# Kernel optimization log

Hardware: AMD Instinct MI355X
Metric: run time of the kernel (lower is better)

The kernel has to match this reference:

```python
import jax, jax.numpy as jnp
import numpy as np

EMBED = 64
ATT_FACTOR = 10
N_FIELDS = 50
BATCH = 2048


def setup_inputs() -> dict:
    key = jax.random.key(0)
    k_x, k_w, k_h, k_p = jax.random.split(key, 4)
    x = jax.random.normal(k_x, (BATCH, N_FIELDS, EMBED), dtype=jnp.float32)
    # xavier-normal-ish init for params
    attention_W = jax.random.normal(k_w, (EMBED, ATT_FACTOR), dtype=jnp.float32) * (2.0 / (EMBED + ATT_FACTOR)) ** 0.5
    attention_b = jnp.zeros((ATT_FACTOR,), dtype=jnp.float32)
    projection_h = jax.random.normal(k_h, (ATT_FACTOR, 1), dtype=jnp.float32) * (2.0 / (ATT_FACTOR + 1)) ** 0.5
    projection_p = jax.random.normal(k_p, (EMBED, 1), dtype=jnp.float32) * (2.0 / (EMBED + 1)) ** 0.5
    return {"x": x, "attention_W": attention_W, "attention_b": attention_b,
            "projection_h": projection_h, "projection_p": projection_p}


def reference(x, attention_W, attention_b, projection_h, projection_p):
    F_ = x.shape[1]
    idx_i, idx_j = np.triu_indices(F_, k=1)  # all pairs (i<j), P = F*(F-1)/2
    inter = x[:, idx_i, :] * x[:, idx_j, :]  # [B, P, E]
    att_tmp = jax.nn.relu(jnp.einsum('bpe,ef->bpf', inter, attention_W) + attention_b)  # [B,P,A]
    logits = jnp.einsum('bpf,fo->bpo', att_tmp, projection_h)  # [B,P,1]
    score = jax.nn.softmax(logits, axis=1)  # softmax over pairs
    att_out = jnp.sum(score * inter, axis=1)  # [B, E]
    # dropout is identity at inference
    return att_out @ projection_p  # [B, 1]
```

## Files before the change

kernel.cpp:

```cpp
#include <hip/hip_runtime.h>
#include <math.h>


#define F_ 50
#define E_ 64
#define A_ 10
#define XDIM 64
#define XSTR 72
#define NT 384

typedef _Float16 half8 __attribute__((ext_vector_type(8)));
typedef _Float16 half4t __attribute__((ext_vector_type(4)));
typedef float f32x16 __attribute__((ext_vector_type(16)));

__global__ __launch_bounds__(NT, 2)
void afm_mfma_kernel(const float* __restrict__ x,
                     const float* __restrict__ W,
                     const float* __restrict__ bias,
                     const float* __restrict__ h,
                     const float* __restrict__ pp,
                     float* __restrict__ out, int nbatch) {
  __shared__ __align__(16) _Float16 sXh[2 * XDIM * XSTR];
  __shared__ __align__(16) _Float16 sWh[(A_ + 1) * E_];
  __shared__ float sb[A_], sh[A_];
  __shared__ float rn[6], rd[6];

  const int tid = threadIdx.x;
  const int b0 = blockIdx.x * 2;

  for (int q = tid; q < 2 * F_ * 16; q += NT) {
    int bb = q >= 800;
    int r4 = q - bb * 800;
    int f = r4 >> 4, e4 = r4 & 15;
    if (b0 + bb < nbatch) {
      float4 v = *(const float4*)(x + (size_t)(b0 + bb) * (F_ * E_) + f * E_ + e4 * 4);
      half4t hv = { (_Float16)v.x, (_Float16)v.y, (_Float16)v.z, (_Float16)v.w };
      *(half4t*)(sXh + bb * (XDIM * XSTR) + f * XSTR + e4 * 4) = hv;
    }
  }
  for (int t = tid; t < 2 * 14 * 16; t += NT) {
    int bb = t >= 224;
    int z = t - bb * 224;
    int f = F_ + (z >> 4), e4 = z & 15;
    half4t zv = { (_Float16)0.f, (_Float16)0.f, (_Float16)0.f, (_Float16)0.f };
    *(half4t*)(sXh + bb * (XDIM * XSTR) + f * XSTR + e4 * 4) = zv;
  }
  if (tid < (A_ + 1) * 32) {
    int kk = tid >> 5, e2 = tid & 31;
    float v0, v1;
    if (kk < A_) { v0 = W[(2 * e2) * A_ + kk]; v1 = W[(2 * e2 + 1) * A_ + kk]; }
    else         { v0 = pp[2 * e2];            v1 = pp[2 * e2 + 1]; }
    sWh[kk * E_ + 2 * e2]     = (_Float16)v0;
    sWh[kk * E_ + 2 * e2 + 1] = (_Float16)v1;
  }
  if (tid < A_) { sb[tid] = bias[tid]; sh[tid] = h[tid]; }
  __syncthreads();

  const int w6 = tid >> 6, lane = tid & 63;
  const int bb = (w6 >= 3), tile = w6 - bb * 3;
  const int m0 = (tile == 2) ? 32 : 0;
  const int n0 = (tile == 0) ? 0 : 32;
  const int row = lane & 31, half = lane >> 5;
  const bool bvalid = (b0 + bb) < nbatch;

  float num = 0.f, den = 0.f;
  if (bvalid) {
    const _Float16* xb = sXh + bb * (XDIM * XSTR);
    half8 axf[4], bxf[4];
#pragma unroll
    for (int es = 0; es < 4; ++es) {
      int eoff = es * 16 + half * 8;
      axf[es] = *(const half8*)(xb + (m0 + row) * XSTR + eoff);
      bxf[es] = *(const half8*)(xb + (n0 + row) * XSTR + eoff);
    }

    f32x16 sacc = {0,0,0,0,0,0,0,0,0,0,0,0,0,0,0,0};
#pragma unroll
    for (int es = 0; es < 4; ++es) {
      half8 pv = *(const half8*)(sWh + A_ * E_ + es * 16 + half * 8);
      sacc = __builtin_amdgcn_mfma_f32_32x32x16_f16(axf[es] * pv, bxf[es], sacc, 0, 0, 0);
    }

    float lg[16];
#pragma unroll
    for (int r = 0; r < 16; ++r) lg[r] = 0.f;
#pragma unroll 1
    for (int k = 0; k < A_; ++k) {
      f32x16 acc = {0,0,0,0,0,0,0,0,0,0,0,0,0,0,0,0};
#pragma unroll
      for (int es = 0; es < 4; ++es) {
        half8 wv = *(const half8*)(sWh + k * E_ + es * 16 + half * 8);
        acc = __builtin_amdgcn_mfma_f32_32x32x16_f16(axf[es] * wv, bxf[es], acc, 0, 0, 0);
      }
      float bk = sb[k], hk = sh[k];
#pragma unroll
      for (int r = 0; r < 16; ++r)
        lg[r] = fmaf(fmaxf(acc[r] + bk, 0.f), hk, lg[r]);
    }

    const int jcol = n0 + row;
#pragma unroll
    for (int r = 0; r < 16; ++r) {
      int irow = m0 + (r & 3) + 8 * (r >> 2) + 4 * half;
      bool valid = (irow < jcol) && (jcol < F_);
      float w = valid ? __expf(lg[r]) : 0.f;
      num = fmaf(w, sacc[r], num);
      den += w;
    }
  }

#pragma unroll
  for (int off = 32; off; off >>= 1) {
    num += __shfl_down(num, off);
    den += __shfl_down(den, off);
  }
  if (lane == 0) { rn[w6] = num; rd[w6] = den; }
  __syncthreads();
  if (tid == 0)
    out[b0] = (rn[0] + rn[1] + rn[2]) / (rd[0] + rd[1] + rd[2]);
  if (tid == 64 && b0 + 1 < nbatch)
    out[b0 + 1] = (rn[3] + rn[4] + rn[5]) / (rd[3] + rd[4] + rd[5]);
}

extern "C" void kernel_launch(void* const* d_in, const int* in_sizes, int n_in,
                              void* d_out, int out_size, void* d_ws, size_t ws_size,
                              hipStream_t stream) {
  const float* x  = (const float*)d_in[0];
  const float* W  = (const float*)d_in[1];
  const float* bb = (const float*)d_in[2];
  const float* h  = (const float*)d_in[3];
  const float* pp = (const float*)d_in[4];
  float* out = (float*)d_out;
  const int nbatch = in_sizes[0] / (F_ * E_);
  const int nblocks = (nbatch + 1) / 2;
  afm_mfma_kernel<<<nblocks, NT, 0, stream>>>(x, W, bb, h, pp, out, nbatch);
}
```

Measured before the change: 95.40 us.

## Use one wave per batch with 16x16 MFMA upper-triangle tiles

```diff
diff --git a/kernel.cpp b/kernel.cpp
--- a/kernel.cpp
+++ b/kernel.cpp
@@ -5,107 +5,139 @@
 #define F_ 50
 #define E_ 64
 #define A_ 10
-#define XDIM 64
 #define XSTR 72
-#define NT 384
+#define NT 256
+#define LOG2E 1.44269504088896f
 
 typedef _Float16 half8 __attribute__((ext_vector_type(8)));
 typedef _Float16 half4t __attribute__((ext_vector_type(4)));
-typedef float f32x16 __attribute__((ext_vector_type(16)));
+typedef float f32x4 __attribute__((ext_vector_type(4)));
 
 __global__ __launch_bounds__(NT, 2)
-void afm_mfma_kernel(const float* __restrict__ x,
-                     const float* __restrict__ W,
-                     const float* __restrict__ bias,
-                     const float* __restrict__ h,
-                     const float* __restrict__ pp,
-                     float* __restrict__ out, int nbatch) {
-  __shared__ __align__(16) _Float16 sXh[2 * XDIM * XSTR];
+void afm_kernel(const float* __restrict__ x,
+                const float* __restrict__ W,
+                const float* __restrict__ bias,
+                const float* __restrict__ h,
+                const float* __restrict__ pp,
+                float* __restrict__ out, int nbatch) {
+  __shared__ __align__(16) _Float16 sXh[4 * 64 * XSTR];
   __shared__ __align__(16) _Float16 sWh[(A_ + 1) * E_];
   __shared__ float sb[A_], sh[A_];
-  __shared__ float rn[6], rd[6];
 
   const int tid = threadIdx.x;
-  const int b0 = blockIdx.x * 2;
+  const int lane = tid & 63, w4 = tid >> 6;
+  const int b = blockIdx.x * 4 + w4;
+  const bool bvalid = b < nbatch;
+  _Float16* xb = sXh + w4 * (64 * XSTR);
 
-  for (int q = tid; q < 2 * F_ * 16; q += NT) {
-    int bb = q >= 800;
-    int r4 = q - bb * 800;
-    int f = r4 >> 4, e4 = r4 & 15;
-    if (b0 + bb < nbatch) {
-      float4 v = *(const float4*)(x + (size_t)(b0 + bb) * (F_ * E_) + f * E_ + e4 * 4);
-      half4t hv = { (_Float16)v.x, (_Float16)v.y, (_Float16)v.z, (_Float16)v.w };
-      *(half4t*)(sXh + bb * (XDIM * XSTR) + f * XSTR + e4 * 4) = hv;
+  if (bvalid) {
+    const float4* xs = (const float4*)(x + (size_t)b * (F_ * E_));
+    for (int q = lane; q < F_ * 16; q += 64) {
+      float4 v = xs[q];
+      int f = q >> 4, e4 = q & 15;
+      half4t hv = {(_Float16)v.x, (_Float16)v.y, (_Float16)v.z, (_Float16)v.w};
+      *(half4t*)(xb + f * XSTR + e4 * 4) = hv;
     }
   }
-  for (int t = tid; t < 2 * 14 * 16; t += NT) {
-    int bb = t >= 224;
-    int z = t - bb * 224;
-    int f = F_ + (z >> 4), e4 = z & 15;
-    half4t zv = { (_Float16)0.f, (_Float16)0.f, (_Float16)0.f, (_Float16)0.f };
-    *(half4t*)(sXh + bb * (XDIM * XSTR) + f * XSTR + e4 * 4) = zv;
+  for (int q = lane; q < 14 * 8; q += 64) {
+    int f = F_ + (q >> 3), c = q & 7;
+    half8 z = {};
+    *(half8*)(xb + f * XSTR + c * 8) = z;
   }
-  if (tid < (A_ + 1) * 32) {
-    int kk = tid >> 5, e2 = tid & 31;
-    float v0, v1;
-    if (kk < A_) { v0 = W[(2 * e2) * A_ + kk]; v1 = W[(2 * e2 + 1) * A_ + kk]; }
-    else         { v0 = pp[2 * e2];            v1 = pp[2 * e2 + 1]; }
-    sWh[kk * E_ + 2 * e2]     = (_Float16)v0;
-    sWh[kk * E_ + 2 * e2 + 1] = (_Float16)v1;
+  if (tid < 11 * 16) {
+    int k = tid >> 4, e4 = tid & 15;
+    float v0, v1, v2, v3;
+    if (k < A_) {
+      v0 = W[(e4 * 4 + 0) * A_ + k]; v1 = W[(e4 * 4 + 1) * A_ + k];
+      v2 = W[(e4 * 4 + 2) * A_ + k]; v3 = W[(e4 * 4 + 3) * A_ + k];
+    } else {
+      float4 t4 = *(const float4*)(pp + e4 * 4);
+      v0 = t4.x; v1 = t4.y; v2 = t4.z; v3 = t4.w;
+    }
+    half4t hv = {(_Float16)v0, (_Float16)v1, (_Float16)v2, (_Float16)v3};
+    *(half4t*)(sWh + k * E_ + e4 * 4) = hv;
   }
-  if (tid < A_) { sb[tid] = bias[tid]; sh[tid] = h[tid]; }
+  if (tid < A_) { sb[tid] = bias[tid]; sh[tid] = h[tid] * LOG2E; }
   __syncthreads();
-
-  const int w6 = tid >> 6, lane = tid & 63;
-  const int bb = (w6 >= 3), tile = w6 - bb * 3;
-  const int m0 = (tile == 2) ? 32 : 0;
-  const int n0 = (tile == 0) ? 0 : 32;
-  const int row = lane & 31, half = lane >> 5;
-  const bool bvalid = (b0 + bb) < nbatch;
 
   float num = 0.f, den = 0.f;
   if (bvalid) {
-    const _Float16* xb = sXh + bb * (XDIM * XSTR);
-    half8 axf[4], bxf[4];
+    const int m = lane & 15, q8 = lane >> 4;
+    half8 fr[4][2];
 #pragma unroll
-    for (int es = 0; es < 4; ++es) {
-      int eoff = es * 16 + half * 8;
-      axf[es] = *(const half8*)(xb + (m0 + row) * XSTR + eoff);
-      bxf[es] = *(const half8*)(xb + (n0 + row) * XSTR + eoff);
+    for (int bi = 0; bi < 4; ++bi)
+#pragma unroll
+      for (int es = 0; es < 2; ++es)
+        fr[bi][es] = *(const half8*)(xb + (bi * 16 + m) * XSTR + es * 32 + q8 * 8);
+
+    float lg[10][4];
+#pragma unroll
+    for (int t0 = 0; t0 < 10; ++t0)
+#pragma unroll
+      for (int r = 0; r < 4; ++r) lg[t0][r] = 0.f;
+
+#pragma unroll 1
+    for (int k = 0; k < A_; ++k) {
+      half8 wv0 = *(const half8*)(sWh + k * E_ + q8 * 8);
+      half8 wv1 = *(const half8*)(sWh + k * E_ + 32 + q8 * 8);
+      float bk = sb[k];
+      f32x4 ci = {bk, bk, bk, bk};
+      half8 sa0[4];
+#pragma unroll
+      for (int bi = 0; bi < 4; ++bi) sa0[bi] = fr[bi][0] * wv0;
+      f32x4 t[10];
+      {
+        int idx = 0;
+#pragma unroll
+        for (int bi = 0; bi < 4; ++bi)
+#pragma unroll
+          for (int bj = bi; bj < 4; ++bj)
+            t[idx++] = __builtin_amdgcn_mfma_f32_16x16x32_f16(sa0[bi], fr[bj][0], ci, 0, 0, 0);
+      }
+      half8 sa1[4];
+#pragma unroll
+      for (int bi = 0; bi < 4; ++bi) sa1[bi] = fr[bi][1] * wv1;
+      {
+        int idx = 0;
+#pragma unroll
+        for (int bi = 0; bi < 4; ++bi)
+#pragma unroll
+          for (int bj = bi; bj < 4; ++bj) {
+            t[idx] = __builtin_amdgcn_mfma_f32_16x16x32_f16(sa1[bi], fr[bj][1], t[idx], 0, 0, 0);
+            ++idx;
+          }
+      }
+      float hk = sh[k];
+#pragma unroll
+      for (int idx = 0; idx < 10; ++idx)
+#pragma unroll
+        for (int r = 0; r < 4; ++r)
+          lg[idx][r] = fmaf(fmaxf(t[idx][r], 0.f), hk, lg[idx][r]);
     }
 
-    f32x16 sacc = {0,0,0,0,0,0,0,0,0,0,0,0,0,0,0,0};
+    half8 pv0 = *(const half8*)(sWh + A_ * E_ + q8 * 8);
+    half8 pv1 = *(const half8*)(sWh + A_ * E_ + 32 + q8 * 8);
+    f32x4 z4 = {0.f, 0.f, 0.f, 0.f};
+    int idx = 0;
 #pragma unroll
-    for (int es = 0; es < 4; ++es) {
-      half8 pv = *(const half8*)(sWh + A_ * E_ + es * 16 + half * 8);
-      sacc = __builtin_amdgcn_mfma_f32_32x32x16_f16(axf[es] * pv, bxf[es], sacc, 0, 0, 0);
-    }
-
-    float lg[16];
+    for (int bi = 0; bi < 4; ++bi) {
+      half8 pa0 = fr[bi][0] * pv0;
+      half8 pa1 = fr[bi][1] * pv1;
 #pragma unroll
-    for (int r = 0; r < 16; ++r) lg[r] = 0.f;
-#pragma unroll 1
-    for (int k = 0; k < A_; ++k) {
-      f32x16 acc = {0,0,0,0,0,0,0,0,0,0,0,0,0,0,0,0};
+      for (int bj = bi; bj < 4; ++bj) {
+        f32x4 s4 = __builtin_amdgcn_mfma_f32_16x16x32_f16(pa0, fr[bj][0], z4, 0, 0, 0);
+        s4 = __builtin_amdgcn_mfma_f32_16x16x32_f16(pa1, fr[bj][1], s4, 0, 0, 0);
 #pragma unroll
-      for (int es = 0; es < 4; ++es) {
-        half8 wv = *(const half8*)(sWh + k * E_ + es * 16 + half * 8);
-        acc = __builtin_amdgcn_mfma_f32_32x32x16_f16(axf[es] * wv, bxf[es], acc, 0, 0, 0);
+        for (int r = 0; r < 4; ++r) {
+          int irow = bi * 16 + q8 * 4 + r;
+          int jcol = bj * 16 + m;
+          bool valid = (irow < jcol) && (jcol < F_);
+          float w = valid ? exp2f(lg[idx][r]) : 0.f;
+          num = fmaf(w, s4[r], num);
+          den += w;
+        }
+        ++idx;
       }
-      float bk = sb[k], hk = sh[k];
-#pragma unroll
-      for (int r = 0; r < 16; ++r)
-        lg[r] = fmaf(fmaxf(acc[r] + bk, 0.f), hk, lg[r]);
-    }
-
-    const int jcol = n0 + row;
-#pragma unroll
-    for (int r = 0; r < 16; ++r) {
-      int irow = m0 + (r & 3) + 8 * (r >> 2) + 4 * half;
-      bool valid = (irow < jcol) && (jcol < F_);
-      float w = valid ? __expf(lg[r]) : 0.f;
-      num = fmaf(w, sacc[r], num);
-      den += w;
     }
   }
 
@@ -114,12 +146,7 @@
     num += __shfl_down(num, off);
     den += __shfl_down(den, off);
   }
-  if (lane == 0) { rn[w6] = num; rd[w6] = den; }
-  __syncthreads();
-  if (tid == 0)
-    out[b0] = (rn[0] + rn[1] + rn[2]) / (rd[0] + rd[1] + rd[2]);
-  if (tid == 64 && b0 + 1 < nbatch)
-    out[b0 + 1] = (rn[3] + rn[4] + rn[5]) / (rd[3] + rd[4] + rd[5]);
+  if (lane == 0 && bvalid) out[b] = num / den;
 }
 
 extern "C" void kernel_launch(void* const* d_in, const int* in_sizes, int n_in,
@@ -132,6 +159,6 @@
   const float* pp = (const float*)d_in[4];
   float* out = (float*)d_out;
   const int nbatch = in_sizes[0] / (F_ * E_);
-  const int nblocks = (nbatch + 1) / 2;
-  afm_mfma_kernel<<<nblocks, NT, 0, stream>>>(x, W, bb, h, pp, out, nbatch);
+  const int nblocks = (nbatch + 3) / 4;
+  afm_kernel<<<nblocks, NT, 0, stream>>>(x, W, bb, h, pp, out, nbatch);
 }
```

Result: faster. 87.92 us (-7.8%).
